# Kernel optimization log

Hardware: AMD Instinct MI355X
Metric: run time of the kernel (lower is better)

Reference implementation:

```python
import jax, jax.numpy as jnp
import numpy as np

B, S, D = 2, 1024, 1024
E, DG, L, H = 8, 256, 3, 2048
THR = 0.3


def setup_inputs() -> dict:
    key = jax.random.key(0)
    ks = jax.random.split(key, 10)
    hidden_states = jax.random.normal(ks[0], (B, S, D), jnp.float32)
    X = jax.random.normal(ks[1], (E, D), jnp.float32) * 0.02          # gate expert embeddings
    W_mlp = jax.random.normal(ks[2], (D, DG), jnp.float32) * (D ** -0.5)
    W_struct = jax.random.normal(ks[3], (D, DG), jnp.float32) * (D ** -0.5)
    conv_W = jax.random.normal(ks[4], (L, DG, DG), jnp.float32) * (DG ** -0.5)
    w_proj = jax.random.normal(ks[5], (DG,), jnp.float32) * (DG ** -0.5)
    W1 = jax.random.normal(ks[6], (E, D, H), jnp.float32) * (D ** -0.5)  # per-expert FFN up
    W2 = jax.random.normal(ks[7], (E, H, D), jnp.float32) * (H ** -0.5)  # per-expert FFN down
    lamb = jnp.asarray(1.5, jnp.float32)
    theta = jnp.asarray([E / 2.0], jnp.float32)
    count = jnp.zeros((E,), jnp.float32)
    # --- structural graph, precomputed once as in GoEgate.get_edges ---
    expn = np.asarray(jax.nn.silu(X @ W_struct))
    expn = expn / np.linalg.norm(expn, axis=1, keepdims=True)
    sim = expn @ expn.T
    y, perc, mask = 1.0, 0.0, None
    while perc < THR:
        mask = np.abs(sim) >= y
        perc = mask.sum() / (E * E)
        y -= 0.01
    N = E + 1  # experts + 1 token node per block
    A = np.zeros((N, N), np.float32)
    A[:E, :E] = mask
    A[:E, E] = 1.0
    A[E, :E] = 1.0
    A = A + np.eye(N, dtype=np.float32)  # GCNConv adds self-loops (experts end at 2, token node at 1)
    dinv = 1.0 / np.sqrt(A.sum(1))
    A_hat = jnp.asarray(dinv[:, None] * A * dinv[None, :])  # D^-1/2 (A+I) D^-1/2, [N, N]
    return dict(hidden_states=hidden_states, X=X, W_mlp=W_mlp, W_struct=W_struct,
                conv_W=conv_W, w_proj=w_proj, W1=W1, W2=W2, lamb=lamb, theta=theta,
                count=count, A_hat=A_hat, top_k=2)


def reference(hidden_states, X, W_mlp, W_struct, conv_W, w_proj, W1, W2,
              lamb, theta, count, A_hat, top_k):
    act = jax.nn.silu
    b, s, d = hidden_states.shape
    x2d = hidden_states.reshape(-1, d)            # [T, D]
    T = x2d.shape[0]
    # ---- GoEgate ----
    xg = act(x2d @ W_mlp)                          # [T, DG]
    expg = act(X @ W_struct)                       # [E, DG]
    node_x = jnp.concatenate(
        [jnp.broadcast_to(expg[None], (T, E, DG)), xg[:, None, :]], axis=1)  # [T, N, DG]
    for l in range(conv_W.shape[0]):
        node_x = act(jnp.einsum('nm,tmg->tng', A_hat, node_x @ conv_W[l]))   # GCN layer
    logits = (node_x @ w_proj)[:, :E]              # drop token-node column -> [T, E]
    probs = jax.nn.softmax(logits, axis=-1)        # router_logits after softmax
    rw, sel = jax.lax.top_k(probs, top_k)          # [T, k]
    # count accumulation (uses un-normalized topk weights)
    cmat = jnp.zeros((T, E), probs.dtype).at[jnp.arange(T)[:, None], sel].add(rw)
    now_count = count + cmat.sum(0) * top_k        # [E]
    rw = rw / rw.sum(-1, keepdims=True)            # normalize routing weights
    w_full = jnp.zeros((T, E), probs.dtype).at[jnp.arange(T)[:, None], sel].add(rw)
    # ---- per-expert FFN dispatch/combine (dense reference) ----
    h = act(jnp.einsum('td,edh->eth', x2d, W1))    # [E, T, H]
    expert_out = jnp.einsum('eth,ehd->etd', h, W2) # [E, T, D]
    final = jnp.einsum('etd,te->td', expert_out, w_full).reshape(b, s, d)
    loss_component = jnp.concatenate(
        [probs, now_count[None, :], jnp.broadcast_to(lamb, (1, E)),
         jnp.broadcast_to(theta, (1, E))], axis=0)  # [T+3, E]
    return final, loss_component
```

## Files before the change

### kernel.cpp

```cpp
#include <hip/hip_runtime.h>
#include <math.h>

#define TT 2048
#define Dm 1024
#define DGc 256
#define Ec 8
#define Nc 9
#define Hc 2048
#define PADMAX 5120
#define NT64MAX 80

typedef __attribute__((ext_vector_type(8))) short short8v;
typedef __attribute__((ext_vector_type(4))) float f32x4;

typedef __attribute__((address_space(1))) const void gvoid;
typedef __attribute__((address_space(3))) void svoid;

__device__ __forceinline__ void gll16(const void* g, void* l) {
    __builtin_amdgcn_global_load_lds((gvoid*)g, (svoid*)l, 16, 0, 0);
}

__device__ __forceinline__ float silu_f(float x) { return x / (1.f + __expf(-x)); }

__device__ __forceinline__ unsigned short bf16_rne(float f) {
    union { float f; unsigned u; } u; u.f = f;
    return (unsigned short)((u.u + 0x7fffu + ((u.u >> 16) & 1u)) >> 16);
}
__device__ __forceinline__ float bf16_to_f(unsigned short h) {
    union { unsigned u; float f; } u; u.u = ((unsigned)h) << 16; return u.f;
}
__device__ __forceinline__ void split2(float x, unsigned short& h, unsigned short& l) {
    h = bf16_rne(x);
    l = bf16_rne(x - bf16_to_f(h));
}

__device__ __forceinline__ void tsplit_body(const float* S, unsigned short* dh,
        unsigned short* dl, int R, int C, int r0, int c0, int tid, float (*t)[36]) {
    int i = tid >> 3, j4 = (tid & 7) * 4;
    *(float4*)&t[i][j4] = *(const float4*)&S[(size_t)(r0 + i) * C + c0 + j4];
    __syncthreads();
    int ci = tid >> 3, r4 = (tid & 7) * 4;
    ushort4 h, l;
    split2(t[r4 + 0][ci], h.x, l.x);
    split2(t[r4 + 1][ci], h.y, l.y);
    split2(t[r4 + 2][ci], h.z, l.z);
    split2(t[r4 + 3][ci], h.w, l.w);
    size_t o = (size_t)(c0 + ci) * R + r0 + r4;
    *(ushort4*)&dh[o] = h;
    *(ushort4*)&dl[o] = l;
}

__global__ __launch_bounds__(256) void k_prep(const float* hs, const float* Wmlp,
        const float* convW, const float* X, const float* Wst,
        const float* count, const float* lamb, const float* theta,
        unsigned short* hs_hi, unsigned short* hs_lo,
        unsigned short* WmT_h, unsigned short* WmT_l,
        unsigned short* WcT_h, unsigned short* WcT_l,
        float* Xpart, float* out, int* tcnt) {
    __shared__ float tbuf[32][36];
    __shared__ float xs[Ec][64];
    int b = blockIdx.x;
    int tid = threadIdx.x;
    if (b < 1024) {
        size_t i = ((size_t)b * 256 + tid) * 8;
        float4 v0 = *(const float4*)&hs[i];
        float4 v1 = *(const float4*)&hs[i + 4];
        ushort4 h0, l0, h1, l1;
        split2(v0.x, h0.x, l0.x); split2(v0.y, h0.y, l0.y);
        split2(v0.z, h0.z, l0.z); split2(v0.w, h0.w, l0.w);
        split2(v1.x, h1.x, l1.x); split2(v1.y, h1.y, l1.y);
        split2(v1.z, h1.z, l1.z); split2(v1.w, h1.w, l1.w);
        *(ushort4*)&hs_hi[i] = h0; *(ushort4*)&hs_hi[i + 4] = h1;
        *(ushort4*)&hs_lo[i] = l0; *(ushort4*)&hs_lo[i + 4] = l1;
    } else if (b < 1280) {
        int i2 = b - 1024;
        tsplit_body(Wmlp, WmT_h, WmT_l, Dm, DGc, (i2 >> 3) * 32, (i2 & 7) * 32, tid, tbuf);
    } else if (b < 1472) {
        int i2 = b - 1280;
        int e = i2 >> 6, rem = i2 & 63;
        tsplit_body(convW + (size_t)e * DGc * DGc, WcT_h + (size_t)e * DGc * DGc,
                    WcT_l + (size_t)e * DGc * DGc, DGc, DGc,
                    (rem >> 3) * 32, (rem & 7) * 32, tid, tbuf);
    } else if (b < 1488) {
        int p = b - 1472;
        int kb = p * 64;
        if (tid < 128) {
            int e = tid >> 4, k4 = (tid & 15) * 4;
            *(float4*)&xs[e][k4] = *(const float4*)&X[(size_t)e * Dm + kb + k4];
        }
        __syncthreads();
        float acc[Ec];
#pragma unroll
        for (int e = 0; e < Ec; e++) acc[e] = 0.f;
#pragma unroll 4
        for (int k = 0; k < 64; k++) {
            float w = Wst[(size_t)(kb + k) * DGc + tid];
#pragma unroll
            for (int e = 0; e < Ec; e++) acc[e] += xs[e][k] * w;
        }
#pragma unroll
        for (int e = 0; e < Ec; e++) Xpart[(size_t)p * Ec * DGc + e * DGc + tid] = acc[e];
    } else {
        if (tid < Ec) {
            float* loss = out + (size_t)TT * Dm;
            loss[(size_t)(TT + 1) * Ec + tid] = lamb[0];
            loss[(size_t)(TT + 2) * Ec + tid] = theta[0];
        }
        for (int i = tid; i < TT; i += 256) tcnt[i] = 0;
    }
}

__global__ __launch_bounds__(256) void k_gA(const float* Xpart, const float* W0,
                                            float* Gpart) {
    int g = threadIdx.x;
    int kb = blockIdx.x * 32;
    __shared__ float xs[Ec][32];
    {
        int m = g >> 5, k = g & 31;
        float s = 0.f;
#pragma unroll
        for (int p = 0; p < 16; p++)
            s += Xpart[(size_t)p * Ec * DGc + m * DGc + kb + k];
        xs[m][k] = silu_f(s);
    }
    __syncthreads();
    float acc[Ec];
#pragma unroll
    for (int e = 0; e < Ec; e++) acc[e] = 0.f;
#pragma unroll 4
    for (int k = 0; k < 32; k++) {
        float w = W0[(size_t)(kb + k) * DGc + g];
#pragma unroll
        for (int e = 0; e < Ec; e++) acc[e] += xs[e][k] * w;
    }
#pragma unroll
    for (int e = 0; e < Ec; e++)
        Gpart[(size_t)blockIdx.x * Ec * DGc + e * DGc + g] = acc[e];
}

__global__ __launch_bounds__(256) void k_s1fin(const float* Gpart, const float* Ahat,
                                               float* S1) {
    int g = threadIdx.x;
    float Gl[Ec];
#pragma unroll
    for (int m = 0; m < Ec; m++) {
        float s = 0.f;
#pragma unroll
        for (int kb = 0; kb < 8; kb++)
            s += Gpart[(size_t)kb * Ec * DGc + m * DGc + g];
        Gl[m] = s;
    }
#pragma unroll
    for (int n = 0; n < Nc; n++) {
        float s = 0.f;
#pragma unroll
        for (int m = 0; m < Ec; m++) s += Ahat[n * Nc + m] * Gl[m];
        S1[n * DGc + g] = s;
    }
}

template<int BM, int KD, int KS, int BK, int EPI>
__global__ __launch_bounds__(256) void gemm4s(const unsigned short* Ah,
        const unsigned short* Al, const unsigned short* Bh, const unsigned short* Bl,
        float* Cf, unsigned short* Oh, unsigned short* Ol) {
    constexpr int FM = BM / 32;
    constexpr int KLEN = KD / KS;
    constexpr int CH = BK / 8;
    constexpr int RPP = 256 / CH;
    constexpr int APASS = BM / RPP;
    constexpr int BPASS = 128 / RPP;
    constexpr int KKS = BK / 32;
    int m0 = blockIdx.x * BM, n0 = blockIdx.y * 128;
    int k0 = blockIdx.z * KLEN;
    __shared__ __align__(16) unsigned short AsH[BM * BK];
    __shared__ __align__(16) unsigned short AsL[BM * BK];
    __shared__ __align__(16) unsigned short BsH[128 * BK];
    __shared__ __align__(16) unsigned short BsL[128 * BK];
    int tid = threadIdx.x, lane = tid & 63, wid = tid >> 6;
    int wr = wid >> 1, wc = wid & 1, lo = lane & 15, hi = lane >> 4;

    f32x4 acc[FM][4];
#pragma unroll
    for (int m = 0; m < FM; m++)
#pragma unroll
        for (int n = 0; n < 4; n++) acc[m][n] = (f32x4)(0.f);

    int arow = tid / CH;
    int cswz = ((tid & (CH - 1)) ^ (arow & (CH - 1))) * 8;
    const unsigned short* AgH = Ah + (size_t)(m0 + arow) * KD + cswz;
    const unsigned short* AgL = Al + (size_t)(m0 + arow) * KD + cswz;
    const unsigned short* BgH = Bh + (size_t)(n0 + arow) * KD + cswz;
    const unsigned short* BgL = Bl + (size_t)(n0 + arow) * KD + cswz;

    for (int kb = k0; kb < k0 + KLEN; kb += BK) {
#pragma unroll
        for (int r = 0; r < APASS; r++) {
            gll16(AgH + (size_t)r * RPP * KD + kb, (char*)AsH + r * 4096 + tid * 16);
            gll16(AgL + (size_t)r * RPP * KD + kb, (char*)AsL + r * 4096 + tid * 16);
        }
#pragma unroll
        for (int r = 0; r < BPASS; r++) {
            gll16(BgH + (size_t)r * RPP * KD + kb, (char*)BsH + r * 4096 + tid * 16);
            gll16(BgL + (size_t)r * RPP * KD + kb, (char*)BsL + r * 4096 + tid * 16);
        }
        __syncthreads();
#pragma unroll
        for (int kk = 0; kk < KKS; kk++) {
            int csel = ((kk * 4 + hi) ^ (lo & (CH - 1))) * 8;
            short8v ah[FM], al[FM], bh[4], bl[4];
#pragma unroll
            for (int m = 0; m < FM; m++) {
                ah[m] = *(const short8v*)&AsH[(wr * (BM / 2) + m * 16 + lo) * BK + csel];
                al[m] = *(const short8v*)&AsL[(wr * (BM / 2) + m * 16 + lo) * BK + csel];
            }
#pragma unroll
            for (int n = 0; n < 4; n++) {
                bh[n] = *(const short8v*)&BsH[(wc * 64 + n * 16 + lo) * BK + csel];
                bl[n] = *(const short8v*)&BsL[(wc * 64 + n * 16 + lo) * BK + csel];
            }
#pragma unroll
            for (int m = 0; m < FM; m++)
#pragma unroll
                for (int n = 0; n < 4; n++)
                    acc[m][n] = __builtin_amdgcn_mfma_f32_16x16x32_bf16(ah[m], bh[n], acc[m][n], 0, 0, 0);
#pragma unroll
            for (int m = 0; m < FM; m++)
#pragma unroll
                for (int n = 0; n < 4; n++)
                    acc[m][n] = __builtin_amdgcn_mfma_f32_16x16x32_bf16(ah[m], bl[n], acc[m][n], 0, 0, 0);
#pragma unroll
            for (int m = 0; m < FM; m++)
#pragma unroll
                for (int n = 0; n < 4; n++)
                    acc[m][n] = __builtin_amdgcn_mfma_f32_16x16x32_bf16(al[m], bh[n], acc[m][n], 0, 0, 0);
        }
        __syncthreads();
    }

#pragma unroll
    for (int m = 0; m < FM; m++) {
#pragma unroll
        for (int n = 0; n < 4; n++) {
            int col = n0 + wc * 64 + n * 16 + lo;
#pragma unroll
            for (int r = 0; r < 4; r++) {
                int row = m0 + wr * (BM / 2) + m * 16 + hi * 4 + r;
                if (EPI == 0) {
                    Cf[(size_t)row * 256 + col] = acc[m][n][r];
                } else if (EPI == 3) {
                    Cf[((size_t)blockIdx.z * TT + row) * 256 + col] = acc[m][n][r];
                } else {
                    float s = silu_f(acc[m][n][r]);
                    unsigned short h, l;
                    split2(s, h, l);
                    Oh[(size_t)row * 256 + col] = h;
                    Ol[(size_t)row * 256 + col] = l;
                }
            }
        }
    }
}

__global__ __launch_bounds__(256) void k_finsplit(const float* src,
        unsigned short* dh, unsigned short* dl) {
    size_t i = ((size_t)blockIdx.x * 256 + threadIdx.x) * 4;
    float4 v0 = *(const float4*)&src[i];
    float4 v1 = *(const float4*)&src[(size_t)TT * DGc + i];
    float4 v2 = *(const float4*)&src[(size_t)2 * TT * DGc + i];
    float4 v3 = *(const float4*)&src[(size_t)3 * TT * DGc + i];
    float4 v = make_float4(v0.x + v1.x + v2.x + v3.x, v0.y + v1.y + v2.y + v3.y,
                           v0.z + v1.z + v2.z + v3.z, v0.w + v1.w + v2.w + v3.w);
    ushort4 h, l;
    split2(silu_f(v.x), h.x, l.x);
    split2(silu_f(v.y), h.y, l.y);
    split2(silu_f(v.z), h.z, l.z);
    split2(silu_f(v.w), h.w, l.w);
    *(ushort4*)&dh[i] = h;
    *(ushort4*)&dl[i] = l;
}

__global__ __launch_bounds__(256) void k_l1(const float* ypart, const float* S1,
        const float* Ahat, unsigned short* nh, unsigned short* nl) {
    int t = blockIdx.x, g = threadIdx.x;
    float yv = ypart[(size_t)t * DGc + g] + ypart[(size_t)TT * DGc + (size_t)t * DGc + g];
#pragma unroll
    for (int n = 0; n < Nc; n++) {
        float c = Ahat[n * Nc + Ec];
        float s = silu_f(S1[n * DGc + g] + c * yv);
        unsigned short h, l;
        split2(s, h, l);
        size_t o = ((size_t)t * Nc + n) * DGc + g;
        nh[o] = h; nl[o] = l;
    }
}

__global__ __launch_bounds__(256) void k_mix2(const float* Z, const float* Ahat,
        unsigned short* nh, unsigned short* nl) {
    int t = blockIdx.x, g = threadIdx.x;
    __shared__ float A[Nc * Nc];
    if (g < Nc * Nc) A[g] = Ahat[g];
    __syncthreads();
    float z[Nc];
#pragma unroll
    for (int m = 0; m < Nc; m++) z[m] = Z[((size_t)t * Nc + m) * DGc + g];
#pragma unroll
    for (int n = 0; n < Nc; n++) {
        float s = 0.f;
#pragma unroll
        for (int m = 0; m < Nc; m++) s += A[n * Nc + m] * z[m];
        s = silu_f(s);
        unsigned short h, l;
        split2(s, h, l);
        size_t o = ((size_t)t * Nc + n) * DGc + g;
        nh[o] = h; nl[o] = l;
    }
}

__global__ __launch_bounds__(256) void k_mix3(const float* Z, const float* Ahat,
        const float* wproj, float* out, int* sel, float* selv) {
    __shared__ float A[Nc * Nc];
    __shared__ float wp[DGc];
    int tid = threadIdx.x;
    if (tid < Nc * Nc) A[tid] = Ahat[tid];
    wp[tid] = wproj[tid];
    __syncthreads();
    int wid = tid >> 6, lane = tid & 63;
    int t = blockIdx.x * 4 + wid;
    float lg[Ec];
#pragma unroll
    for (int e = 0; e < Ec; e++) lg[e] = 0.f;
#pragma unroll
    for (int j = 0; j < 4; j++) {
        int g = j * 64 + lane;
        float z[Nc];
#pragma unroll
        for (int m = 0; m < Nc; m++) z[m] = Z[((size_t)t * Nc + m) * DGc + g];
#pragma unroll
        for (int e = 0; e < Ec; e++) {
            float s = 0.f;
#pragma unroll
            for (int m = 0; m < Nc; m++) s += A[e * Nc + m] * z[m];
            lg[e] += silu_f(s) * wp[g];
        }
    }
#pragma unroll
    for (int off = 32; off >= 1; off >>= 1) {
#pragma unroll
        for (int e = 0; e < Ec; e++) lg[e] += __shfl_xor(lg[e], off);
    }
    if (lane == 0) {
        float mx = -1e30f;
#pragma unroll
        for (int e = 0; e < Ec; e++) mx = fmaxf(mx, lg[e]);
        float pr[Ec], s = 0.f;
#pragma unroll
        for (int e = 0; e < Ec; e++) { pr[e] = __expf(lg[e] - mx); s += pr[e]; }
        float inv = 1.f / s;
        float* lrow = out + (size_t)TT * Dm + (size_t)t * Ec;
#pragma unroll
        for (int e = 0; e < Ec; e++) { pr[e] *= inv; lrow[e] = pr[e]; }
        int i0 = 0; float v0 = pr[0];
#pragma unroll
        for (int e = 1; e < Ec; e++) if (pr[e] > v0) { v0 = pr[e]; i0 = e; }
        int i1 = -1; float v1 = -1e30f;
#pragma unroll
        for (int e = 0; e < Ec; e++) if (e != i0 && pr[e] > v1) { v1 = pr[e]; i1 = e; }
        sel[t * 2] = i0; sel[t * 2 + 1] = i1;
        selv[t * 2] = v0; selv[t * 2 + 1] = v1;
    }
}

__global__ __launch_bounds__(256) void k_route(const int* sel, const float* selv,
        const float* count, float* out, int* cnt, int* toklist, float* wlist) {
    int e = blockIdx.x;
    int tid = threadIdx.x;
    __shared__ int sc[256];
    __shared__ float sw[256];
    __shared__ int sbase;
    __shared__ float swtot;
    if (tid == 0) { sbase = 0; swtot = 0.f; }
    __syncthreads();
    for (int c = 0; c < TT; c += 256) {
        int t = c + tid;
        int i0 = sel[t * 2], i1 = sel[t * 2 + 1];
        float v0 = selv[t * 2], v1 = selv[t * 2 + 1];
        int f = 0; float vraw = 0.f;
        if (i0 == e) { f = 1; vraw = v0; }
        else if (i1 == e) { f = 1; vraw = v1; }
        float winv = 1.f / (v0 + v1);
        sc[tid] = f;
        sw[tid] = 2.f * vraw;
        __syncthreads();
        for (int off = 1; off < 256; off <<= 1) {
            int a = (tid >= off) ? sc[tid - off] : 0;
            float b = (tid >= off) ? sw[tid - off] : 0.f;
            __syncthreads();
            sc[tid] += a; sw[tid] += b;
            __syncthreads();
        }
        if (f) {
            int pos = sbase + sc[tid] - 1;
            toklist[e * TT + pos] = t;
            wlist[e * TT + pos] = vraw * winv;
        }
        __syncthreads();
        if (tid == 255) { sbase += sc[255]; swtot += sw[255]; }
        __syncthreads();
    }
    if (tid == 0) {
        cnt[e] = sbase;
        out[(size_t)TT * Dm + (size_t)TT * Ec + e] = count[e] + swtot;
    }
}

__global__ __launch_bounds__(256) void k_tcast(const float* src, unsigned short* dst,
                                               int R, int C) {
    int e = blockIdx.z;
    int c0 = blockIdx.x * 32, r0 = blockIdx.y * 32;
    const float* S = src + (size_t)e * R * C;
    unsigned short* Dq = dst + (size_t)e * R * C;
    __shared__ float t[32][36];
    int tid = threadIdx.x;
    int i = tid >> 3, j4 = (tid & 7) * 4;
    *(float4*)&t[i][j4] = *(const float4*)&S[(size_t)(r0 + i) * C + c0 + j4];
    __syncthreads();
    int ci = tid >> 3, r4 = (tid & 7) * 4;
    ushort4 v;
    v.x = bf16_rne(t[r4 + 0][ci]);
    v.y = bf16_rne(t[r4 + 1][ci]);
    v.z = bf16_rne(t[r4 + 2][ci]);
    v.w = bf16_rne(t[r4 + 3][ci]);
    *(ushort4*)&Dq[(size_t)(c0 + ci) * R + r0 + r4] = v;
}

__global__ void k_offs(const int* cnt, int* poffs, int* tile_e, int* tile_m0) {
    if (threadIdx.x == 0) {
        int pad = 0, nt = 0;
        for (int e = 0; e < Ec; e++) {
            poffs[e] = pad;
            int te = (cnt[e] + 63) >> 6;
            for (int i = 0; i < te; i++) { tile_e[nt] = e; tile_m0[nt] = pad + i * 64; nt++; }
            pad += te * 64;
        }
        poffs[Ec] = pad;
        for (; nt < NT64MAX; nt++) { tile_e[nt] = -1; tile_m0[nt] = 0; }
    }
}

__global__ __launch_bounds__(256) void k_gather(const unsigned short* hs_hi,
        const int* cnt, const int* poffs, const int* toklist, const float* wlist,
        unsigned short* xb, int* tcnt, int* tok2slot, float* tok2w) {
    int tid = threadIdx.x;
    int s = blockIdx.x * 2 + (tid >> 7);
    int j = (tid & 127) * 8;
    int e = 0;
#pragma unroll
    for (int q = 1; q < Ec; q++) if (s >= poffs[q]) e = q;
    int pos = s - poffs[e];
    int tok = -1; float w = 0.f;
    if (pos < cnt[e]) { tok = toklist[e * TT + pos]; w = wlist[e * TT + pos]; }
    if (j == 0 && tok >= 0) {
        int idx = atomicAdd(&tcnt[tok], 1);
        tok2slot[tok * 2 + idx] = s;
        tok2w[tok * 2 + idx] = w;
    }
    short8v o;
    if (tok >= 0) {
        o = *(const short8v*)&hs_hi[(size_t)tok * Dm + j];
    } else {
        o = (short8v)(short)0;
    }
    *(short8v*)&xb[(size_t)s * Dm + j] = o;
}

template<int KDIM, int NDIM, int MODE, int KS>
__global__ __launch_bounds__(256) void k_mfma(const unsigned short* Abuf,
        const unsigned short* Wt, const int* tile_e, const int* tile_m0,
        unsigned short* outp) {
    constexpr int NY = NDIM / 128;
    constexpr int KLEN = KDIM / KS;
    constexpr int CPX = (NT64MAX * NY * KS) / 8;
    int bid = blockIdx.x;
    int flat = (bid & 7) * CPX + (bid >> 3);
    int tx = flat / (NY * KS);
    int rem = flat % (NY * KS);
    int y = rem / KS, ks = rem % KS;
    int e = tile_e[tx];
    if (e < 0) return;
    int m0 = tile_m0[tx];
    int n0 = y * 128;
    int k0 = ks * KLEN;
    __shared__ __align__(16) unsigned short As[64 * 128];
    __shared__ __align__(16) unsigned short Bs[128 * 128];
    int tid = threadIdx.x;
    int lane = tid & 63;
    int wid = tid >> 6;
    int wr = wid >> 1, wc = wid & 1;
    int lo = lane & 15, hi = lane >> 4;

    f32x4 acc[2][4];
#pragma unroll
    for (int m = 0; m < 2; m++)
#pragma unroll
        for (int n = 0; n < 4; n++) acc[m][n] = (f32x4)(0.f);

    int arow = tid >> 4;
    int cswz = ((tid & 15) ^ (arow & 15)) * 8;
    const unsigned short* Ag = Abuf + (size_t)(m0 + arow) * KDIM + cswz;
    const unsigned short* Bg = Wt + (size_t)e * NDIM * KDIM
                               + (size_t)(n0 + arow) * KDIM + cswz;

    for (int kb = k0; kb < k0 + KLEN; kb += 128) {
#pragma unroll
        for (int r = 0; r < 4; r++)
            gll16(Ag + (size_t)r * 16 * KDIM + kb, (char*)As + r * 4096 + tid * 16);
#pragma unroll
        for (int r = 0; r < 8; r++)
            gll16(Bg + (size_t)r * 16 * KDIM + kb, (char*)Bs + r * 4096 + tid * 16);
        __syncthreads();
#pragma unroll
        for (int kk = 0; kk < 4; kk++) {
            int csel = ((kk * 4 + hi) ^ lo) * 8;
            short8v a[2], b[4];
#pragma unroll
            for (int m = 0; m < 2; m++)
                a[m] = *(const short8v*)&As[(wr * 32 + m * 16 + lo) * 128 + csel];
#pragma unroll
            for (int n = 0; n < 4; n++)
                b[n] = *(const short8v*)&Bs[(wc * 64 + n * 16 + lo) * 128 + csel];
#pragma unroll
            for (int m = 0; m < 2; m++)
#pragma unroll
                for (int n = 0; n < 4; n++)
                    acc[m][n] = __builtin_amdgcn_mfma_f32_16x16x32_bf16(a[m], b[n], acc[m][n], 0, 0, 0);
        }
        __syncthreads();
    }

#pragma unroll
    for (int m = 0; m < 2; m++) {
#pragma unroll
        for (int n = 0; n < 4; n++) {
            int col = n0 + wc * 64 + n * 16 + lo;
#pragma unroll
            for (int r = 0; r < 4; r++) {
                int row = m0 + wr * 32 + m * 16 + hi * 4 + r;
                if (MODE == 0) {
                    outp[(size_t)row * NDIM + col] = bf16_rne(silu_f(acc[m][n][r]));
                } else {
                    outp[((size_t)ks * PADMAX + row) * Dm + col] = bf16_rne(acc[m][n][r]);
                }
            }
        }
    }
}

__global__ __launch_bounds__(256) void k_combine(const unsigned short* Opart,
        const int* tok2slot, const float* tok2w, float* out) {
    int t = blockIdx.x, tid = threadIdx.x;
    int s0 = tok2slot[t * 2], s1 = tok2slot[t * 2 + 1];
    float w0 = tok2w[t * 2], w1 = tok2w[t * 2 + 1];
    int c = tid * 4;
    ushort4 a0 = *(const ushort4*)&Opart[(size_t)s0 * Dm + c];
    ushort4 a1 = *(const ushort4*)&Opart[((size_t)PADMAX + s0) * Dm + c];
    ushort4 b0 = *(const ushort4*)&Opart[(size_t)s1 * Dm + c];
    ushort4 b1 = *(const ushort4*)&Opart[((size_t)PADMAX + s1) * Dm + c];
    float4 r;
    r.x = w0 * (bf16_to_f(a0.x) + bf16_to_f(a1.x)) + w1 * (bf16_to_f(b0.x) + bf16_to_f(b1.x));
    r.y = w0 * (bf16_to_f(a0.y) + bf16_to_f(a1.y)) + w1 * (bf16_to_f(b0.y) + bf16_to_f(b1.y));
    r.z = w0 * (bf16_to_f(a0.z) + bf16_to_f(a1.z)) + w1 * (bf16_to_f(b0.z) + bf16_to_f(b1.z));
    r.w = w0 * (bf16_to_f(a0.w) + bf16_to_f(a1.w)) + w1 * (bf16_to_f(b0.w) + bf16_to_f(b1.w));
    *(float4*)&out[(size_t)t * Dm + c] = r;
}

extern "C" void kernel_launch(void* const* d_in, const int* in_sizes, int n_in,
                              void* d_out, int out_size, void* d_ws, size_t ws_size,
                              hipStream_t stream) {
    const float* hs    = (const float*)d_in[0];
    const float* X     = (const float*)d_in[1];
    const float* Wmlp  = (const float*)d_in[2];
    const float* Wst   = (const float*)d_in[3];
    const float* convW = (const float*)d_in[4];
    const float* wproj = (const float*)d_in[5];
    const float* W1    = (const float*)d_in[6];
    const float* W2    = (const float*)d_in[7];
    const float* lamb  = (const float*)d_in[8];
    const float* theta = (const float*)d_in[9];
    const float* count = (const float*)d_in[10];
    const float* Ahat  = (const float*)d_in[11];
    float* out = (float*)d_out;
    char* ws = (char*)d_ws;

    int*            cnt     = (int*)(ws + 8192);
    int*            poffs   = (int*)(ws + 8320);
    int*            tile_e  = (int*)(ws + 8448);
    int*            tile_m0 = (int*)(ws + 8960);
    float*          S1      = (float*)(ws + 9728);
    int*            toklist = (int*)(ws + 20480);
    float*          wlist   = (float*)(ws + 86016);
    int*            tcnt    = (int*)(ws + 151552);
    int*            tok2slot= (int*)(ws + 159744);
    float*          tok2w   = (float*)(ws + 176128);
    int*            sel     = (int*)(ws + 192512);
    float*          selv    = (float*)(ws + 208896);
    unsigned short* xb      = (unsigned short*)(ws + 237568);
    unsigned short* W1T     = (unsigned short*)(ws + 10723328);
    unsigned short* W2T     = (unsigned short*)(ws + 44277760);
    unsigned short* hb      = (unsigned short*)(ws + 77832192);
    unsigned short* Opart   = W1T;

    char* G = ws + 10723328;
    unsigned short* hs_hi = (unsigned short*)(G);
    unsigned short* hs_lo = (unsigned short*)(G + 4194304);
    unsigned short* WmT_h = (unsigned short*)(G + 8388608);
    unsigned short* WmT_l = (unsigned short*)(G + 8912896);
    unsigned short* WcT_h = (unsigned short*)(G + 9437184);
    unsigned short* WcT_l = (unsigned short*)(G + 9830400);
    unsigned short* xg_h  = (unsigned short*)(G + 10223616);
    unsigned short* xg_l  = (unsigned short*)(G + 11272192);
    float*          ypart = (float*)(G + 12320768);
    unsigned short* n_h   = (unsigned short*)(G + 16515072);
    unsigned short* n_l   = (unsigned short*)(G + 25952256);
    float*          Zb    = (float*)(G + 35389440);
    float*          Gpart = (float*)(G + 54263808);
    float*          xgp   = (float*)(G + 54329344);
    float*          Xpart = (float*)(G + 62717952);


    k_prep<<<1489, 256, 0, stream>>>(hs, Wmlp, convW, X, Wst, count, lamb, theta,
                                     hs_hi, hs_lo, WmT_h, WmT_l, WcT_h, WcT_l,
                                     Xpart, out, tcnt);
    k_gA<<<DGc / 32, 256, 0, stream>>>(Xpart, convW, Gpart);
    k_s1fin<<<1, 256, 0, stream>>>(Gpart, Ahat, S1);
    gemm4s<64, Dm, 4, 128, 3><<<dim3(TT / 64, 2, 4), 256, 0, stream>>>(
        hs_hi, hs_lo, WmT_h, WmT_l, xgp, nullptr, nullptr);
    k_finsplit<<<TT * DGc / 1024, 256, 0, stream>>>(xgp, xg_h, xg_l);
    gemm4s<64, DGc, 2, 128, 3><<<dim3(TT / 64, 2, 2), 256, 0, stream>>>(
        xg_h, xg_l, WcT_h, WcT_l, ypart, nullptr, nullptr);
    k_l1<<<TT, 256, 0, stream>>>(ypart, S1, Ahat, n_h, n_l);
    gemm4s<64, DGc, 1, 64, 0><<<dim3(TT * Nc / 64, 2, 1), 256, 0, stream>>>(
        n_h, n_l, WcT_h + 65536, WcT_l + 65536, Zb, nullptr, nullptr);
    k_mix2<<<TT, 256, 0, stream>>>(Zb, Ahat, n_h, n_l);
    gemm4s<64, DGc, 1, 64, 0><<<dim3(TT * Nc / 64, 2, 1), 256, 0, stream>>>(
        n_h, n_l, WcT_h + 131072, WcT_l + 131072, Zb, nullptr, nullptr);
    k_mix3<<<TT / 4, 256, 0, stream>>>(Zb, Ahat, wproj, out, sel, selv);
    k_route<<<Ec, 256, 0, stream>>>(sel, selv, count, out, cnt, toklist, wlist);
    k_offs<<<1, 1, 0, stream>>>(cnt, poffs, tile_e, tile_m0);
    k_gather<<<PADMAX / 2, 256, 0, stream>>>(hs_hi, cnt, poffs, toklist, wlist,
                                             xb, tcnt, tok2slot, tok2w);
    k_tcast<<<dim3(Hc / 32, Dm / 32, Ec), 256, 0, stream>>>(W1, W1T, Dm, Hc);
    k_tcast<<<dim3(Dm / 32, Hc / 32, Ec), 256, 0, stream>>>(W2, W2T, Hc, Dm);
    k_mfma<Dm, Hc, 0, 1><<<NT64MAX * (Hc / 128), 256, 0, stream>>>(
        xb, W1T, tile_e, tile_m0, hb);
    k_mfma<Hc, Dm, 1, 2><<<NT64MAX * (Dm / 128) * 2, 256, 0, stream>>>(
        hb, W2T, tile_e, tile_m0, Opart);
    k_combine<<<TT, 256, 0, stream>>>(Opart, tok2slot, tok2w, out);
}
```

Measured before the change: 209.1 us.

## Fold W1/W2 transpose-cast into prep, drop k_offs, shrink MFMA K-tile

Moves the W1/W2 bf16 transpose-cast into the k_prep launch, so it runs alongside the gate prologue when the workspace is large enough to keep separate buffers. Wider 32x128 slabs replace the 32x32 tiles. The single-thread k_offs kernel is removed, and each gather/MFMA block now derives its expert and offset inline from cnt. The MFMA K-step drops from 128 to 64 to halve LDS use and raise occupancy, at the cost of more syncs per tile.

```diff
diff --git a/kernel.cpp b/kernel.cpp
--- a/kernel.cpp
+++ b/kernel.cpp
@@ -50,15 +50,52 @@
     *(ushort4*)&dl[o] = l;
 }
 
+__device__ __forceinline__ void tcslab_body(const float* S, unsigned short* D,
+        int R, int C, int r0, int c0, int tid, float* sb ) {
+    int r = tid >> 3;
+    int c16 = (tid & 7) * 16;
+#pragma unroll
+    for (int q = 0; q < 4; q++) {
+        float4 v = *(const float4*)&S[(size_t)(r0 + r) * C + c0 + c16 + q * 4];
+        *(float4*)&sb[r * 132 + c16 + q * 4] = v;
+    }
+    __syncthreads();
+    int ci = tid >> 1;
+    int h16 = (tid & 1) * 16;
+#pragma unroll
+    for (int q = 0; q < 4; q++) {
+        ushort4 o;
+        o.x = bf16_rne(sb[(h16 + q * 4 + 0) * 132 + ci]);
+        o.y = bf16_rne(sb[(h16 + q * 4 + 1) * 132 + ci]);
+        o.z = bf16_rne(sb[(h16 + q * 4 + 2) * 132 + ci]);
+        o.w = bf16_rne(sb[(h16 + q * 4 + 3) * 132 + ci]);
+        *(ushort4*)&D[(size_t)(c0 + ci) * R + r0 + h16 + q * 4] = o;
+    }
+}
+
+__global__ __launch_bounds__(256) void k_tcslab(const float* src, unsigned short* dst,
+                                                int R, int C) {
+    __shared__ float sb[32 * 132];
+    int per = (R / 32) * (C / 128);
+    int e = blockIdx.x / per;
+    int rem = blockIdx.x % per;
+    int cpr = C / 128;
+    int r0 = (rem / cpr) * 32;
+    int c0 = (rem % cpr) * 128;
+    tcslab_body(src + (size_t)e * R * C, dst + (size_t)e * R * C, R, C, r0, c0,
+                threadIdx.x, sb);
+}
+
 __global__ __launch_bounds__(256) void k_prep(const float* hs, const float* Wmlp,
         const float* convW, const float* X, const float* Wst,
         const float* count, const float* lamb, const float* theta,
         unsigned short* hs_hi, unsigned short* hs_lo,
         unsigned short* WmT_h, unsigned short* WmT_l,
         unsigned short* WcT_h, unsigned short* WcT_l,
-        float* Xpart, float* out, int* tcnt) {
-    __shared__ float tbuf[32][36];
-    __shared__ float xs[Ec][64];
+        float* Xpart, float* out, int* tcnt,
+        const float* W1, const float* W2,
+        unsigned short* W1T, unsigned short* W2T) {
+    __shared__ float sbuf[32 * 132];
     int b = blockIdx.x;
     int tid = threadIdx.x;
     if (b < 1024) {
@@ -74,14 +111,16 @@
         *(ushort4*)&hs_lo[i] = l0; *(ushort4*)&hs_lo[i + 4] = l1;
     } else if (b < 1280) {
         int i2 = b - 1024;
-        tsplit_body(Wmlp, WmT_h, WmT_l, Dm, DGc, (i2 >> 3) * 32, (i2 & 7) * 32, tid, tbuf);
+        tsplit_body(Wmlp, WmT_h, WmT_l, Dm, DGc, (i2 >> 3) * 32, (i2 & 7) * 32,
+                    tid, (float(*)[36])sbuf);
     } else if (b < 1472) {
         int i2 = b - 1280;
         int e = i2 >> 6, rem = i2 & 63;
         tsplit_body(convW + (size_t)e * DGc * DGc, WcT_h + (size_t)e * DGc * DGc,
                     WcT_l + (size_t)e * DGc * DGc, DGc, DGc,
-                    (rem >> 3) * 32, (rem & 7) * 32, tid, tbuf);
+                    (rem >> 3) * 32, (rem & 7) * 32, tid, (float(*)[36])sbuf);
     } else if (b < 1488) {
+        float (*xs)[64] = (float(*)[64])sbuf;
         int p = b - 1472;
         int kb = p * 64;
         if (tid < 128) {
@@ -100,13 +139,27 @@
         }
 #pragma unroll
         for (int e = 0; e < Ec; e++) Xpart[(size_t)p * Ec * DGc + e * DGc + tid] = acc[e];
-    } else {
+    } else if (b == 1488) {
         if (tid < Ec) {
             float* loss = out + (size_t)TT * Dm;
             loss[(size_t)(TT + 1) * Ec + tid] = lamb[0];
             loss[(size_t)(TT + 2) * Ec + tid] = theta[0];
         }
         for (int i = tid; i < TT; i += 256) tcnt[i] = 0;
+    } else {
+        int i = b - 1489;
+        if (i < 4096) {
+            int e = i >> 9, rem = i & 511;
+            int r0 = (rem >> 4) * 32, c0 = (rem & 15) * 128;
+            tcslab_body(W1 + (size_t)e * Dm * Hc, W1T + (size_t)e * Dm * Hc,
+                        Dm, Hc, r0, c0, tid, sbuf);
+        } else {
+            i -= 4096;
+            int e = i >> 9, rem = i & 511;
+            int r0 = (rem >> 3) * 32, c0 = (rem & 7) * 128;
+            tcslab_body(W2 + (size_t)e * Hc * Dm, W2T + (size_t)e * Hc * Dm,
+                        Hc, Dm, r0, c0, tid, sbuf);
+        }
     }
 }
 
@@ -413,52 +466,22 @@
     }
 }
 
-__global__ __launch_bounds__(256) void k_tcast(const float* src, unsigned short* dst,
-                                               int R, int C) {
-    int e = blockIdx.z;
-    int c0 = blockIdx.x * 32, r0 = blockIdx.y * 32;
-    const float* S = src + (size_t)e * R * C;
-    unsigned short* Dq = dst + (size_t)e * R * C;
-    __shared__ float t[32][36];
-    int tid = threadIdx.x;
-    int i = tid >> 3, j4 = (tid & 7) * 4;
-    *(float4*)&t[i][j4] = *(const float4*)&S[(size_t)(r0 + i) * C + c0 + j4];
-    __syncthreads();
-    int ci = tid >> 3, r4 = (tid & 7) * 4;
-    ushort4 v;
-    v.x = bf16_rne(t[r4 + 0][ci]);
-    v.y = bf16_rne(t[r4 + 1][ci]);
-    v.z = bf16_rne(t[r4 + 2][ci]);
-    v.w = bf16_rne(t[r4 + 3][ci]);
-    *(ushort4*)&Dq[(size_t)(c0 + ci) * R + r0 + r4] = v;
-}
-
-__global__ void k_offs(const int* cnt, int* poffs, int* tile_e, int* tile_m0) {
-    if (threadIdx.x == 0) {
-        int pad = 0, nt = 0;
-        for (int e = 0; e < Ec; e++) {
-            poffs[e] = pad;
-            int te = (cnt[e] + 63) >> 6;
-            for (int i = 0; i < te; i++) { tile_e[nt] = e; tile_m0[nt] = pad + i * 64; nt++; }
-            pad += te * 64;
-        }
-        poffs[Ec] = pad;
-        for (; nt < NT64MAX; nt++) { tile_e[nt] = -1; tile_m0[nt] = 0; }
-    }
-}
-
 __global__ __launch_bounds__(256) void k_gather(const unsigned short* hs_hi,
-        const int* cnt, const int* poffs, const int* toklist, const float* wlist,
+        const int* cnt, const int* toklist, const float* wlist,
         unsigned short* xb, int* tcnt, int* tok2slot, float* tok2w) {
     int tid = threadIdx.x;
     int s = blockIdx.x * 2 + (tid >> 7);
     int j = (tid & 127) * 8;
-    int e = 0;
-#pragma unroll
-    for (int q = 1; q < Ec; q++) if (s >= poffs[q]) e = q;
-    int pos = s - poffs[e];
+    int e = -1, pos = 0, pad = 0, ce = 0;
+#pragma unroll
+    for (int q = 0; q < Ec; q++) {
+        int cq = cnt[q];
+        int span = ((cq + 63) >> 6) * 64;
+        if (e < 0 && s < pad + span) { e = q; pos = s - pad; ce = cq; }
+        pad += span;
+    }
     int tok = -1; float w = 0.f;
-    if (pos < cnt[e]) { tok = toklist[e * TT + pos]; w = wlist[e * TT + pos]; }
+    if (e >= 0 && pos < ce) { tok = toklist[e * TT + pos]; w = wlist[e * TT + pos]; }
     if (j == 0 && tok >= 0) {
         int idx = atomicAdd(&tcnt[tok], 1);
         tok2slot[tok * 2 + idx] = s;
@@ -475,8 +498,7 @@
 
 template<int KDIM, int NDIM, int MODE, int KS>
 __global__ __launch_bounds__(256) void k_mfma(const unsigned short* Abuf,
-        const unsigned short* Wt, const int* tile_e, const int* tile_m0,
-        unsigned short* outp) {
+        const unsigned short* Wt, const int* cnt, unsigned short* outp) {
     constexpr int NY = NDIM / 128;
     constexpr int KLEN = KDIM / KS;
     constexpr int CPX = (NT64MAX * NY * KS) / 8;
@@ -485,13 +507,18 @@
     int tx = flat / (NY * KS);
     int rem = flat % (NY * KS);
     int y = rem / KS, ks = rem % KS;
-    int e = tile_e[tx];
+    int e = -1, m0 = 0, acc_t = 0, pad = 0;
+#pragma unroll
+    for (int q = 0; q < Ec; q++) {
+        int te = (cnt[q] + 63) >> 6;
+        if (e < 0 && tx < acc_t + te) { e = q; m0 = pad + (tx - acc_t) * 64; }
+        acc_t += te; pad += te * 64;
+    }
     if (e < 0) return;
-    int m0 = tile_m0[tx];
     int n0 = y * 128;
     int k0 = ks * KLEN;
-    __shared__ __align__(16) unsigned short As[64 * 128];
-    __shared__ __align__(16) unsigned short Bs[128 * 128];
+    __shared__ __align__(16) unsigned short As[64 * 64];
+    __shared__ __align__(16) unsigned short Bs[128 * 64];
     int tid = threadIdx.x;
     int lane = tid & 63;
     int wid = tid >> 6;
@@ -504,30 +531,30 @@
 #pragma unroll
         for (int n = 0; n < 4; n++) acc[m][n] = (f32x4)(0.f);
 
-    int arow = tid >> 4;
-    int cswz = ((tid & 15) ^ (arow & 15)) * 8;
-    const unsigned short* Ag = Abuf + (size_t)(m0 + arow) * KDIM + cswz;
+    int arow = tid >> 3;
+    int cswz = ((tid & 7) ^ (arow & 7)) * 8;
+    const unsigned short* Ag = Abuf + (size_t)(m0 + arow) * KDIM + k0 + cswz;
     const unsigned short* Bg = Wt + (size_t)e * NDIM * KDIM
-                               + (size_t)(n0 + arow) * KDIM + cswz;
-
-    for (int kb = k0; kb < k0 + KLEN; kb += 128) {
-#pragma unroll
-        for (int r = 0; r < 4; r++)
-            gll16(Ag + (size_t)r * 16 * KDIM + kb, (char*)As + r * 4096 + tid * 16);
-#pragma unroll
-        for (int r = 0; r < 8; r++)
-            gll16(Bg + (size_t)r * 16 * KDIM + kb, (char*)Bs + r * 4096 + tid * 16);
-        __syncthreads();
-#pragma unroll
-        for (int kk = 0; kk < 4; kk++) {
-            int csel = ((kk * 4 + hi) ^ lo) * 8;
+                               + (size_t)(n0 + arow) * KDIM + k0 + cswz;
+
+    for (int kb = 0; kb < KLEN; kb += 64) {
+        gll16(Ag + kb,                          (char*)As + tid * 16);
+        gll16(Ag + 32 * (size_t)KDIM + kb,      (char*)As + 4096 + tid * 16);
+        gll16(Bg + kb,                          (char*)Bs + tid * 16);
+        gll16(Bg + 32 * (size_t)KDIM + kb,      (char*)Bs + 4096 + tid * 16);
+        gll16(Bg + 64 * (size_t)KDIM + kb,      (char*)Bs + 8192 + tid * 16);
+        gll16(Bg + 96 * (size_t)KDIM + kb,      (char*)Bs + 12288 + tid * 16);
+        __syncthreads();
+#pragma unroll
+        for (int kk = 0; kk < 2; kk++) {
+            int csel = ((kk * 4 + hi) ^ (lo & 7)) * 8;
             short8v a[2], b[4];
 #pragma unroll
             for (int m = 0; m < 2; m++)
-                a[m] = *(const short8v*)&As[(wr * 32 + m * 16 + lo) * 128 + csel];
+                a[m] = *(const short8v*)&As[(wr * 32 + m * 16 + lo) * 64 + csel];
 #pragma unroll
             for (int n = 0; n < 4; n++)
-                b[n] = *(const short8v*)&Bs[(wc * 64 + n * 16 + lo) * 128 + csel];
+                b[n] = *(const short8v*)&Bs[(wc * 64 + n * 16 + lo) * 64 + csel];
 #pragma unroll
             for (int m = 0; m < 2; m++)
 #pragma unroll
@@ -592,9 +619,6 @@
     char* ws = (char*)d_ws;
 
     int*            cnt     = (int*)(ws + 8192);
-    int*            poffs   = (int*)(ws + 8320);
-    int*            tile_e  = (int*)(ws + 8448);
-    int*            tile_m0 = (int*)(ws + 8960);
     float*          S1      = (float*)(ws + 9728);
     int*            toklist = (int*)(ws + 20480);
     float*          wlist   = (float*)(ws + 86016);
@@ -609,7 +633,8 @@
     unsigned short* hb      = (unsigned short*)(ws + 77832192);
     unsigned short* Opart   = W1T;
 
-    char* G = ws + 10723328;
+    bool big = ws_size >= (size_t)174063616;
+    char* G = big ? (ws + 98803712) : (ws + 10723328);
     unsigned short* hs_hi = (unsigned short*)(G);
     unsigned short* hs_lo = (unsigned short*)(G + 4194304);
     unsigned short* WmT_h = (unsigned short*)(G + 8388608);
@@ -626,10 +651,11 @@
     float*          xgp   = (float*)(G + 54329344);
     float*          Xpart = (float*)(G + 62717952);
 
-
-    k_prep<<<1489, 256, 0, stream>>>(hs, Wmlp, convW, X, Wst, count, lamb, theta,
-                                     hs_hi, hs_lo, WmT_h, WmT_l, WcT_h, WcT_l,
-                                     Xpart, out, tcnt);
+    int prep_blocks = big ? (1489 + 8192) : 1489;
+    k_prep<<<prep_blocks, 256, 0, stream>>>(hs, Wmlp, convW, X, Wst, count, lamb,
+                                            theta, hs_hi, hs_lo, WmT_h, WmT_l,
+                                            WcT_h, WcT_l, Xpart, out, tcnt,
+                                            W1, W2, W1T, W2T);
     k_gA<<<DGc / 32, 256, 0, stream>>>(Xpart, convW, Gpart);
     k_s1fin<<<1, 256, 0, stream>>>(Gpart, Ahat, S1);
     gemm4s<64, Dm, 4, 128, 3><<<dim3(TT / 64, 2, 4), 256, 0, stream>>>(
@@ -645,14 +671,15 @@
         n_h, n_l, WcT_h + 131072, WcT_l + 131072, Zb, nullptr, nullptr);
     k_mix3<<<TT / 4, 256, 0, stream>>>(Zb, Ahat, wproj, out, sel, selv);
     k_route<<<Ec, 256, 0, stream>>>(sel, selv, count, out, cnt, toklist, wlist);
-    k_offs<<<1, 1, 0, stream>>>(cnt, poffs, tile_e, tile_m0);
-    k_gather<<<PADMAX / 2, 256, 0, stream>>>(hs_hi, cnt, poffs, toklist, wlist,
+    k_gather<<<PADMAX / 2, 256, 0, stream>>>(hs_hi, cnt, toklist, wlist,
                                              xb, tcnt, tok2slot, tok2w);
-    k_tcast<<<dim3(Hc / 32, Dm / 32, Ec), 256, 0, stream>>>(W1, W1T, Dm, Hc);
-    k_tcast<<<dim3(Dm / 32, Hc / 32, Ec), 256, 0, stream>>>(W2, W2T, Hc, Dm);
+    if (!big) {
+        k_tcslab<<<Ec * (Dm / 32) * (Hc / 128), 256, 0, stream>>>(W1, W1T, Dm, Hc);
+        k_tcslab<<<Ec * (Hc / 32) * (Dm / 128), 256, 0, stream>>>(W2, W2T, Hc, Dm);
+    }
     k_mfma<Dm, Hc, 0, 1><<<NT64MAX * (Hc / 128), 256, 0, stream>>>(
-        xb, W1T, tile_e, tile_m0, hb);
+        xb, W1T, cnt, hb);
     k_mfma<Hc, Dm, 1, 2><<<NT64MAX * (Dm / 128) * 2, 256, 0, stream>>>(
-        hb, W2T, tile_e, tile_m0, Opart);
+        hb, W2T, cnt, Opart);
     k_combine<<<TT, 256, 0, stream>>>(Opart, tok2slot, tok2w, out);
 }
```

Measured after the change: 198.3 us. 5.2% less time.
